# Performance work log

Measured on AMD Instinct MI355X. Metric: run time of the kernel, lower is better.

## Reference

```python
import jax, jax.numpy as jnp
import numpy as np

B, R, N, M, K = 4, 4, 4096, 64, 3
F_NUM = 512
KN = K * N


def _block(x, Ws, bs):
    """SO-Net PointResNet: 1x1 convs + ReLU; last layer sees concat(input, hidden)."""
    h = x
    for W, b in zip(Ws[:-1], bs[:-1]):
        h = jax.nn.relu(jnp.einsum('oc,bcn->bon', W, h) + b[None, :, None])
    h = jnp.concatenate([x, h], axis=1)
    return jax.nn.relu(jnp.einsum('oc,bcn->bon', Ws[-1], h) + bs[-1][None, :, None])


def _forward(x, intensity, node, node_knn_I, fpW, fpB, gpW, gpB):
    # --- som.query_topk: k nearest SOM nodes per point ---
    xd = jax.lax.stop_gradient(x)
    dist = jnp.sum((xd[:, :, :, None] - node[:, :, None, :]) ** 2, axis=1)      # B,N,M
    _, topk = jax.lax.top_k(-dist, K)                                           # B,N,K
    min_idx = topk.transpose(0, 2, 1).reshape(B, KN)                            # B,KN (k copies stacked)
    mask = jax.nn.one_hot(min_idx, M, dtype=jnp.float32)                        # B,KN,M
    mask_row_max = jnp.max(mask, axis=1) > 0                                    # B,M  node has >=1 point
    mask_row_sum = jnp.sum(mask, axis=1)                                        # B,M  points per node

    x_stack = jnp.tile(x, (1, 1, K))                                            # B,2,KN
    cluster_mean = jnp.einsum('bcn,bnm->bcm', jax.lax.stop_gradient(x_stack), mask) \
                   / (mask_row_sum[:, None, :] + 1e-5)                          # B,2,M (detached)

    # --- rotation group (2x2 rotations at angles 2*pi*r/R) ---
    theta = 2.0 * jnp.pi * jnp.arange(R, dtype=jnp.float32) / R
    c, s = jnp.cos(theta), jnp.sin(theta)
    rot = jnp.stack([jnp.stack([c, -s], -1), jnp.stack([s, c], -1)], -2)        # R,2,2

    x_rot = jnp.einsum('rij,bjn->brin', rot, x_stack)                           # B,R,2,KN
    node_rot = jnp.einsum('rij,bjm->brim', rot, cluster_mean)                   # B,R,2,M
    centers = jnp.take_along_axis(node_rot, min_idx[:, None, None, :], axis=3)  # B,R,2,KN
    x_dec = jax.lax.stop_gradient(x_rot - centers).reshape(B * R, 2, KN)

    # --- first PointResNet over all B*R rotation copies ---
    feat = _block(x_dec, fpW, fpB)                                              # BR,128,KN

    # --- index_max scatter-max per SOM cluster (value of argmax == segment max) ---
    seg = jnp.tile(min_idx[:, None, :], (1, R, 1)).reshape(B * R, KN)
    segmax = jax.vmap(lambda f, sgi: jax.ops.segment_max(f.T, sgi, num_segments=M).T)(feat, seg)
    rowmax = jnp.tile(mask_row_max[:, None, :], (1, R, 1)).reshape(B * R, M)
    pooled = jnp.where(rowmax[:, None, :], segmax, feat[:, :, 0:1])             # BR,128,M (empty -> gather idx 0)

    # --- final PointResNet over SOM nodes, then max over nodes and rotations ---
    g_in = jnp.concatenate([node_rot.reshape(B * R, 2, M), pooled], axis=1)     # BR,130,M
    out = _block(g_in, gpW, gpB)                                                # BR,F,M
    return out.reshape(B, R, F_NUM, M).max(axis=3).max(axis=1)                  # B,F


def setup_inputs() -> dict:
    key = jax.random.key(0)
    ks = jax.random.split(key, 24)
    d = {}
    d['x'] = jax.random.normal(ks[0], (B, 2, N), jnp.float32)
    d['intensity'] = jax.random.uniform(ks[1], (B, 1, N), jnp.float32)
    d['node'] = jax.random.normal(ks[2], (B, 2, M), jnp.float32)
    d['node_knn_I'] = jax.random.randint(ks[3], (B, M, 1), 0, M)
    dims_fp = [(64, 2), (64, 64), (128, 64), (128, 130)]      # PointResNet(2,[64,64,128,128])
    dims_gp = [(256, 130), (256, 256), (512, 256), (F_NUM, 642)]  # PointResNet(130,[256,256,512,F])
    i = 4
    for name, dims in (('fp', dims_fp), ('gp', dims_gp)):
        for j, (o, ci) in enumerate(dims):
            d[f'{name}_W{j}'] = jax.random.normal(ks[i], (o, ci), jnp.float32) / np.sqrt(ci).astype(np.float32)
            d[f'{name}_b{j}'] = jnp.zeros((o,), jnp.float32)
            i += 1
    return d


def reference(x, intensity, node, node_knn_I,
              fp_W0, fp_b0, fp_W1, fp_b1, fp_W2, fp_b2, fp_W3, fp_b3,
              gp_W0, gp_b0, gp_W1, gp_b1, gp_W2, gp_b2, gp_W3, gp_b3):
    return _forward(x, intensity, node, node_knn_I,
                    [fp_W0, fp_W1, fp_W2, fp_W3], [fp_b0, fp_b1, fp_b2, fp_b3],
                    [gp_W0, gp_W1, gp_W2, gp_W3], [gp_b0, gp_b1, gp_b2, gp_b3])
```

## Files before the change

kernel.cpp:

```cpp
#include <hip/hip_runtime.h>
#include <stdint.h>

#define BB 4
#define RR 4
#define NN 4096
#define MM 64
#define KK 3
#define KNN 12288
#define BRR 16
#define FF 512

typedef short bf16x8 __attribute__((ext_vector_type(8)));
typedef float f32x4 __attribute__((ext_vector_type(4)));

__device__ __forceinline__ float bf2f(unsigned int u) {
  union { unsigned int i; float f; } v; v.i = u << 16; return v.f;
}
__device__ __forceinline__ unsigned short f2bf(float f) {
  union { float f; unsigned int i; } v; v.f = f;
  unsigned int x = v.i;
  return (unsigned short)((x + 0x7fffu + ((x >> 16) & 1u)) >> 16);
}
__device__ __forceinline__ unsigned int cvtpk(float a, float b) {
  unsigned int r;
  asm("v_cvt_pk_bf16_f32 %0, %1, %2" : "=v"(r) : "v"(a), "v"(b));
  return r;
}
__device__ __forceinline__ float ldf(const void* p, long i, int isbf) {
  if (isbf) return bf2f(((const unsigned short*)p)[i]);
  return ((const float*)p)[i];
}
__device__ __forceinline__ int hsw(int col, int so) { return col * 72  + (so ^ (col & 24)); }
__device__ __forceinline__ int csw(int col, int so) { return col * 136 + (so ^ (col & 24)); }

struct WPtrs { const void* p[7]; };

__global__ __launch_bounds__(256) void k_front(
    const void* __restrict__ x, const void* __restrict__ node, WPtrs wp,
    int* __restrict__ flag, unsigned short* __restrict__ Wb,
    int* __restrict__ idx, float* __restrict__ csum, int* __restrict__ blkcnt) {
  __shared__ int bad;
  __shared__ float nd[2][64];
  __shared__ float cs[192];
  int tid = threadIdx.x;
  if (tid == 0) bad = 0;
  __syncthreads();
  {
    const unsigned short* xs = (const unsigned short*)x;
    int cnt = 0;
    for (int i = tid; i < 1024; i += 256) {
      unsigned short u = xs[i * 2];
      int e = (u >> 7) & 0xFF;
      if (e >= 0x90 || (e > 0 && e <= 0x50)) ++cnt;
    }
    atomicAdd(&bad, cnt);
  }
  __syncthreads();
  int isbf = (bad < 100) ? 1 : 0;
  if (blockIdx.x == 0 && tid == 0) flag[0] = isbf;

  if (blockIdx.x < 2295) {
    const int e0=4096, e1=12288, e2=28928, e3=62208, e4=127744, e5=258816, e6=587520;
    int t = blockIdx.x * 256 + tid;
    if (t >= e6) return;
    int s, base;
    if      (t < e0) { s=0; base=0;  }
    else if (t < e1) { s=1; base=e0; }
    else if (t < e2) { s=2; base=e1; }
    else if (t < e3) { s=3; base=e2; }
    else if (t < e4) { s=4; base=e3; }
    else if (t < e5) { s=5; base=e4; }
    else             { s=6; base=e5; }
    int local = t - base;
    unsigned short u;
    if (isbf) u = ((const unsigned short*)wp.p[s])[local];
    else      u = f2bf(((const float*)wp.p[s])[local]);
    Wb[t] = u;
    return;
  }
  int bi = blockIdx.x - 2295;
  int b = bi >> 4;
  int n = ((bi & 15) << 8) + tid;
  if (tid < 128) nd[tid >> 6][tid & 63] = ldf(node, b * 128 + tid, isbf);
  if (tid < 192) cs[tid] = 0.f;
  __syncthreads();
  float x0 = ldf(x, b * 8192 + n, isbf);
  float x1 = ldf(x, b * 8192 + 4096 + n, isbf);
  float d0 = 1e30f, d1 = 1e30f, d2 = 1e30f;
  int m0 = 0, m1 = 0, m2 = 0;
#pragma unroll 8
  for (int m = 0; m < 64; ++m) {
    float dx = x0 - nd[0][m];
    float dy = x1 - nd[1][m];
    float d = __fmul_rn(dx, dx) + __fmul_rn(dy, dy);
    if (d < d0)      { d2=d1; m2=m1; d1=d0; m1=m0; d0=d; m0=m; }
    else if (d < d1) { d2=d1; m2=m1; d1=d;  m1=m; }
    else if (d < d2) { d2=d;  m2=m; }
  }
  long base = ((long)b * NN + n) * 3;
  idx[base] = m0; idx[base + 1] = m1; idx[base + 2] = m2;
  atomicAdd(&cs[m0*3+0], x0); atomicAdd(&cs[m0*3+1], x1); atomicAdd(&cs[m0*3+2], 1.f);
  atomicAdd(&cs[m1*3+0], x0); atomicAdd(&cs[m1*3+1], x1); atomicAdd(&cs[m1*3+2], 1.f);
  atomicAdd(&cs[m2*3+0], x0); atomicAdd(&cs[m2*3+1], x1); atomicAdd(&cs[m2*3+2], 1.f);
  __syncthreads();
  if (tid < 192) atomicAdd(&csum[b * 192 + tid], cs[tid]);
  if (tid < 64) blkcnt[bi * 64 + tid] = (int)cs[tid*3 + 2];
}

__global__ __launch_bounds__(256) void k_scatter2(
    const float* __restrict__ csum, const int* __restrict__ blkcnt,
    const int* __restrict__ idx, int* __restrict__ sorted,
    float* __restrict__ noderot, int* __restrict__ rowflag) {
  __shared__ int scnt[64];
  __shared__ int soff[64];
  __shared__ int lc[64];
  int tid = threadIdx.x;
  int blk = blockIdx.x;
  int b = blk >> 4, chunk = blk & 15;
  if (tid < 64) scnt[tid] = (int)csum[b*192 + tid*3 + 2];
  __syncthreads();
  if (tid < 64) {
    int m = tid, acc = 0;
    for (int mm = 0; mm < m; ++mm) acc += scnt[mm];
    for (int c = 0; c < chunk; ++c) acc += blkcnt[(b*16 + c)*64 + m];
    soff[m] = acc;
    lc[m] = 0;
    if (chunk == 0) {
      float s0 = csum[b*192 + m*3], s1 = csum[b*192 + m*3 + 1], cc = csum[b*192 + m*3 + 2];
      float mx = s0 / (cc + 1e-5f);
      float my = s1 / (cc + 1e-5f);
      rowflag[b*64 + m] = (cc > 0.f) ? 1 : 0;
      for (int r = 0; r < 4; ++r) {
        float th = 1.5707964f * (float)r;
        float cr = cosf(th), sr = sinf(th);
        noderot[((b*4 + r)*2 + 0)*64 + m] = cr*mx - sr*my;
        noderot[((b*4 + r)*2 + 1)*64 + m] = sr*mx + cr*my;
      }
    }
  }
  __syncthreads();
  int n = ((blk & 15) << 8) + tid;
#pragma unroll
  for (int kk = 0; kk < 3; ++kk) {
    int m = idx[((long)b * NN + n) * 3 + kk];
    int pos = atomicAdd(&lc[m], 1);
    sorted[b * KNN + soff[m] + pos] = (m << 12) | n;
  }
}

__global__ __launch_bounds__(256) void k_fused(
    const void* __restrict__ x, const int* __restrict__ sorted,
    const int* __restrict__ idx, const float* __restrict__ noderot,
    const int* __restrict__ flag,
    const void* __restrict__ fW0, const void* __restrict__ fb0,
    const unsigned short* __restrict__ Wb,
    const void* __restrict__ fb1, const void* __restrict__ fb2,
    const void* __restrict__ fb3,
    unsigned int* __restrict__ pooled, float* __restrict__ feat0) {
  __shared__ unsigned short Cs[64 * 136];
  __shared__ unsigned short Hs[64 * 72];
  __shared__ int mcol[64];
  const unsigned short* fW1 = Wb;
  const unsigned short* fW2 = Wb + 4096;
  const unsigned short* fW3 = Wb + 12288;
  int isbf = flag[0];
  int tid = threadIdx.x, lane = tid & 63, wv = tid >> 6;
  int quad = lane >> 4, lr = lane & 15;
  int br = blockIdx.y, b = br >> 2, r = br & 3;
  if (tid < 64) {
    int e = sorted[b * KNN + blockIdx.x * 64 + tid];
    int m = e >> 12, n = e & 4095;
    int isz = (n == 0 && m == idx[(long)b * NN * 3]) ? 256 : 0;
    mcol[tid] = m | isz;
    float x0 = ldf(x, b*8192 + n, isbf), x1 = ldf(x, b*8192 + 4096 + n, isbf);
    float th = 1.5707964f * (float)r;
    float cr = cosf(th), sr = sinf(th);
    float xd0 = (cr*x0 - sr*x1) - noderot[(br*2 + 0)*64 + m];
    float xd1 = (sr*x0 + cr*x1) - noderot[(br*2 + 1)*64 + m];
    *(unsigned int*)&Cs[csw(tid, 0)] = cvtpk(xd0, xd1);
  }
  __syncthreads();
  {
    int col = tid & 63, og = (tid >> 6) << 4;
    unsigned int xu = *(unsigned int*)&Cs[csw(col, 0)];
    float fx0 = bf2f(xu & 0xffff), fx1 = bf2f(xu >> 16);
    float hv[16];
#pragma unroll
    for (int j = 0; j < 16; ++j) {
      int o = og + j;
      float h = ldf(fb0, o, isbf) + ldf(fW0, o*2, isbf) * fx0 + ldf(fW0, o*2+1, isbf) * fx1;
      hv[j] = fmaxf(h, 0.f);
    }
    union { bf16x8 v; unsigned int u[4]; } o8[2];
#pragma unroll
    for (int j = 0; j < 16; j += 2) o8[j >> 3].u[(j & 7) >> 1] = cvtpk(hv[j], hv[j+1]);
    *(bf16x8*)&Hs[hsw(col, og)]     = o8[0].v;
    *(bf16x8*)&Hs[hsw(col, og + 8)] = o8[1].v;
  }
  __syncthreads();
  {
    int o0 = wv * 16;
    f32x4 acc[4];
    float bb4[4];
#pragma unroll
    for (int rr = 0; rr < 4; ++rr) bb4[rr] = ldf(fb1, o0 + quad*4 + rr, isbf);
#pragma unroll
    for (int nt = 0; nt < 4; ++nt) acc[nt] = (f32x4){bb4[0], bb4[1], bb4[2], bb4[3]};
#pragma unroll
    for (int ks = 0; ks < 64; ks += 32) {
      bf16x8 a = *(const bf16x8*)(fW1 + (o0 + lr)*64 + ks + quad*8);
#pragma unroll
      for (int nt = 0; nt < 4; ++nt) {
        bf16x8 bf = *(bf16x8*)&Hs[hsw(nt*16 + lr, ks + quad*8)];
        acc[nt] = __builtin_amdgcn_mfma_f32_16x16x32_bf16(a, bf, acc[nt], 0, 0, 0);
      }
    }
    __syncthreads();
#pragma unroll
    for (int nt = 0; nt < 4; ++nt) {
      int col = nt*16 + lr;
      unsigned int lo = cvtpk(fmaxf(acc[nt][0], 0.f), fmaxf(acc[nt][1], 0.f));
      unsigned int hi = cvtpk(fmaxf(acc[nt][2], 0.f), fmaxf(acc[nt][3], 0.f));
      *(unsigned long long*)&Hs[hsw(col, o0 + quad*4)] =
          (unsigned long long)lo | ((unsigned long long)hi << 32);
    }
  }
  __syncthreads();
#pragma unroll
  for (int p2 = 0; p2 < 2; ++p2) {
    int o0 = p2*64 + wv*16;
    f32x4 acc[4];
    float bb4[4];
#pragma unroll
    for (int rr = 0; rr < 4; ++rr) bb4[rr] = ldf(fb2, o0 + quad*4 + rr, isbf);
#pragma unroll
    for (int nt = 0; nt < 4; ++nt) acc[nt] = (f32x4){bb4[0], bb4[1], bb4[2], bb4[3]};
#pragma unroll
    for (int ks = 0; ks < 64; ks += 32) {
      bf16x8 a = *(const bf16x8*)(fW2 + (o0 + lr)*64 + ks + quad*8);
#pragma unroll
      for (int nt = 0; nt < 4; ++nt) {
        bf16x8 bf = *(bf16x8*)&Hs[hsw(nt*16 + lr, ks + quad*8)];
        acc[nt] = __builtin_amdgcn_mfma_f32_16x16x32_bf16(a, bf, acc[nt], 0, 0, 0);
      }
    }
#pragma unroll
    for (int nt = 0; nt < 4; ++nt) {
      int col = nt*16 + lr;
      int o = o0 + quad*4;
      unsigned int w0 = cvtpk(fmaxf(acc[nt][0], 0.f), fmaxf(acc[nt][1], 0.f));
      unsigned int w1 = cvtpk(fmaxf(acc[nt][2], 0.f), fmaxf(acc[nt][3], 0.f));
      int so0 = 2 + o;
      int so1 = 4 + o;
      *(unsigned int*)&Cs[csw(col, so0)] = w0;
      *(unsigned int*)&Cs[(so1 < 128) ? csw(col, so1) : (col*136 + so1)] = w1;
    }
  }
  __syncthreads();
  f32x4 acc3[2][4];
#pragma unroll
  for (int p3 = 0; p3 < 2; ++p3) {
    int o0 = p3*64 + wv*16;
    float bb4[4];
#pragma unroll
    for (int rr = 0; rr < 4; ++rr) bb4[rr] = ldf(fb3, o0 + quad*4 + rr, isbf);
#pragma unroll
    for (int nt = 0; nt < 4; ++nt) acc3[p3][nt] = (f32x4){bb4[0], bb4[1], bb4[2], bb4[3]};
#pragma unroll
    for (int ks = 0; ks < 128; ks += 32) {
      union { bf16x8 v; unsigned int u[4]; } au;
      const unsigned int* ap = (const unsigned int*)(fW3 + (long)(o0 + lr)*130 + ks + quad*8);
      au.u[0] = ap[0]; au.u[1] = ap[1]; au.u[2] = ap[2]; au.u[3] = ap[3];
#pragma unroll
      for (int nt = 0; nt < 4; ++nt) {
        bf16x8 bf = *(bf16x8*)&Cs[csw(nt*16 + lr, ks + quad*8)];
        acc3[p3][nt] = __builtin_amdgcn_mfma_f32_16x16x32_bf16(au.v, bf, acc3[p3][nt], 0, 0, 0);
      }
    }
#pragma unroll
    for (int rr = 0; rr < 4; ++rr) {
      int o = o0 + quad*4 + rr;
      unsigned int wu = *(const unsigned int*)(fW3 + (long)o*130 + 128);
      float w0 = bf2f(wu & 0xffff), w1 = bf2f(wu >> 16);
#pragma unroll
      for (int nt = 0; nt < 4; ++nt) {
        unsigned int bu = *(unsigned int*)&Cs[(nt*16 + lr)*136 + 128];
        acc3[p3][nt][rr] += w0 * bf2f(bu & 0xffff) + w1 * bf2f(bu >> 16);
      }
    }
  }
  __syncthreads();
#pragma unroll
  for (int p3 = 0; p3 < 2; ++p3) {
    int o0 = p3*64 + wv*16;
#pragma unroll
    for (int nt = 0; nt < 4; ++nt) {
      int col = nt*16 + lr;
      unsigned int lo = cvtpk(fmaxf(acc3[p3][nt][0], 0.f), fmaxf(acc3[p3][nt][1], 0.f));
      unsigned int hi = cvtpk(fmaxf(acc3[p3][nt][2], 0.f), fmaxf(acc3[p3][nt][3], 0.f));
      *(unsigned long long*)&Cs[csw(col, o0 + quad*4)] =
          (unsigned long long)lo | ((unsigned long long)hi << 32);
    }
  }
  __syncthreads();
  {
    int o = tid & 127, h = tid >> 7;
    int c0 = h * 32;
    int curm = mcol[c0] & 255;
    float v = 0.f;
    for (int c = c0; c < c0 + 32; ++c) {
      int mc = mcol[c];
      int mm = mc & 255;
      float f = bf2f(Cs[csw(c, o)]);
      if (mm != curm) {
        atomicMax(&pooled[(((long)br*64 + curm) << 7) + o], __float_as_uint(v));
        curm = mm; v = 0.f;
      }
      v = fmaxf(v, f);
      if (mc & 256) feat0[br*128 + o] = f;
    }
    atomicMax(&pooled[(((long)br*64 + curm) << 7) + o], __float_as_uint(v));
  }
}

__global__ __launch_bounds__(256) void k_finalize(
    const unsigned int* __restrict__ pooled, const float* __restrict__ feat0,
    const int* __restrict__ rowflag, const float* __restrict__ noderot,
    unsigned short* __restrict__ AG) {
  int t = blockIdx.x * 256 + threadIdx.x;
  int col = t >> 7, o = t & 127;
  int br = col >> 6, m = col & 63, b = br >> 2;
  float v = __uint_as_float(pooled[((long)col << 7) + o]);
  if (!rowflag[b*64 + m]) v = feat0[br*128 + o];
  AG[(long)col*648 + 2 + o] = f2bf(v);
  if (o < 2) AG[(long)col*648 + o] = f2bf(noderot[(br*2 + o)*64 + m]);
}

template<int KW, int KMAIN, bool REM2, int BSTR, int OSTR, int OOFF, int EPI>
__global__ __launch_bounds__(256) void k_gemm(
    const unsigned short* __restrict__ W, const void* __restrict__ bias,
    const int* __restrict__ flag,
    const unsigned short* __restrict__ Bb, unsigned short* __restrict__ Out,
    unsigned int* __restrict__ outmax) {
  int isbf = flag[0];
  int lane = threadIdx.x & 63;
  int wv = threadIdx.x >> 6;
  int quad = lane >> 4, lr = lane & 15;
  int o0 = blockIdx.y * 64 + wv * 16;
  long p0 = (long)blockIdx.x * 64;
  float bia[4];
#pragma unroll
  for (int rr = 0; rr < 4; ++rr) bia[rr] = ldf(bias, o0 + quad*4 + rr, isbf);
  f32x4 acc[4];
#pragma unroll
  for (int nt = 0; nt < 4; ++nt) acc[nt] = (f32x4){bia[0], bia[1], bia[2], bia[3]};
  const unsigned short* arow = W + (long)(o0 + lr) * KW;
  for (int ks = 0; ks < KMAIN; ks += 32) {
    bf16x8 a;
    if constexpr ((KW % 8) == 0) {
      a = *(const bf16x8*)(arow + ks + quad*8);
    } else {
      union { bf16x8 v; unsigned int u[4]; } au;
      const unsigned int* ap = (const unsigned int*)(arow + ks + quad*8);
      au.u[0] = ap[0]; au.u[1] = ap[1]; au.u[2] = ap[2]; au.u[3] = ap[3];
      a = au.v;
    }
#pragma unroll
    for (int nt = 0; nt < 4; ++nt) {
      bf16x8 bf = *(const bf16x8*)(Bb + (p0 + nt*16 + lr) * BSTR + ks + quad*8);
      acc[nt] = __builtin_amdgcn_mfma_f32_16x16x32_bf16(a, bf, acc[nt], 0, 0, 0);
    }
  }
  if constexpr (REM2) {
#pragma unroll
    for (int rr = 0; rr < 4; ++rr) {
      int o = o0 + quad*4 + rr;
      unsigned int wu = *(const unsigned int*)(W + (long)o * KW + KMAIN);
      float w0 = bf2f(wu & 0xffff), w1 = bf2f(wu >> 16);
#pragma unroll
      for (int nt = 0; nt < 4; ++nt) {
        long p = p0 + nt*16 + lr;
        unsigned int bu = *(const unsigned int*)(Bb + p * BSTR + KMAIN);
        acc[nt][rr] += w0 * bf2f(bu & 0xffff) + w1 * bf2f(bu >> 16);
      }
    }
  }
  if constexpr (EPI == 0) {
#pragma unroll
    for (int nt = 0; nt < 4; ++nt) {
      long p = p0 + nt*16 + lr;
      unsigned int lo = cvtpk(fmaxf(acc[nt][0], 0.f), fmaxf(acc[nt][1], 0.f));
      unsigned int hi = cvtpk(fmaxf(acc[nt][2], 0.f), fmaxf(acc[nt][3], 0.f));
      unsigned short* op = Out + p * OSTR + OOFF + o0 + quad*4;
      if constexpr (((OOFF * 2) % 8) == 0) {
        *(unsigned long long*)op = (unsigned long long)lo | ((unsigned long long)hi << 32);
      } else {
        *(unsigned int*)op       = lo;
        *(unsigned int*)(op + 2) = hi;
      }
    }
  } else {
#pragma unroll
    for (int rr = 0; rr < 4; ++rr) {
      float v = fmaxf(fmaxf(acc[0][rr], acc[1][rr]), fmaxf(acc[2][rr], acc[3][rr]));
      v = fmaxf(v, 0.f);
      v = fmaxf(v, __shfl_xor(v, 1, 64));
      v = fmaxf(v, __shfl_xor(v, 2, 64));
      v = fmaxf(v, __shfl_xor(v, 4, 64));
      v = fmaxf(v, __shfl_xor(v, 8, 64));
      if (lr == 0) {
        int bb2 = (int)(blockIdx.x >> 2);
        atomicMax(&outmax[bb2 * FF + o0 + quad*4 + rr], __float_as_uint(v));
      }
    }
  }
}

__global__ __launch_bounds__(256) void k_out(
    const unsigned int* __restrict__ outmax, const int* __restrict__ flag,
    void* __restrict__ out) {
  int t = blockIdx.x * 256 + threadIdx.x;
  float v = __uint_as_float(outmax[t]);
  if (flag[0]) ((unsigned short*)out)[t] = f2bf(v);
  else         ((float*)out)[t] = v;
}

extern "C" void kernel_launch(void* const* d_in, const int* in_sizes, int n_in,
                              void* d_out, int out_size, void* d_ws, size_t ws_size,
                              hipStream_t stream) {
  const void* x    = d_in[0];
  const void* node = d_in[2];
  const void* fpW0 = d_in[4];  const void* fpb0 = d_in[5];
  const void* fpW1 = d_in[6];  const void* fpb1 = d_in[7];
  const void* fpW2 = d_in[8];  const void* fpb2 = d_in[9];
  const void* fpW3 = d_in[10]; const void* fpb3 = d_in[11];
  const void* gpW0 = d_in[12]; const void* gpb0 = d_in[13];
  const void* gpW1 = d_in[14]; const void* gpb1 = d_in[15];
  const void* gpW2 = d_in[16]; const void* gpb2 = d_in[17];
  const void* gpW3 = d_in[18]; const void* gpb3 = d_in[19];

  char* ws = (char*)d_ws;
  int*            flag    = (int*)(ws + 0);
  float*          csum    = (float*)(ws + 256);
  unsigned int*   outmax  = (unsigned int*)(ws + 3328);
  unsigned int*   pooled  = (unsigned int*)(ws + 11520);
  int*            idx     = (int*)(ws + 535808);
  int*            blkcnt  = (int*)(ws + 732416);
  float*          noderot = (float*)(ws + 766208);
  int*            rowflag = (int*)(ws + 774400);
  int*            sorted  = (int*)(ws + 775424);
  float*          feat0   = (float*)(ws + 972032);
  unsigned short* AG      = (unsigned short*)(ws + 980224);
  unsigned short* Hg1     = (unsigned short*)(ws + 2307328);
  unsigned short* Hg2     = (unsigned short*)(ws + 2831616);
  unsigned short* Wb      = (unsigned short*)(ws + 3355904);

  hipMemsetAsync(ws, 0, 535808, stream);

  WPtrs wp; wp.p[0]=fpW1; wp.p[1]=fpW2; wp.p[2]=fpW3; wp.p[3]=gpW0;
  wp.p[4]=gpW1; wp.p[5]=gpW2; wp.p[6]=gpW3;
  k_front<<<2359, 256, 0, stream>>>(x, node, wp, flag, Wb, idx, csum, blkcnt);
  k_scatter2<<<64, 256, 0, stream>>>(csum, blkcnt, idx, sorted, noderot, rowflag);
  k_fused<<<dim3(192, 16), 256, 0, stream>>>(x, sorted, idx, noderot, flag,
                                             fpW0, fpb0, Wb, fpb1, fpb2, fpb3,
                                             pooled, feat0);
  k_finalize<<<512, 256, 0, stream>>>(pooled, feat0, rowflag, noderot, AG);

  const unsigned short* gW0 = Wb + 28928;
  const unsigned short* gW1 = Wb + 62208;
  const unsigned short* gW2 = Wb + 127744;
  const unsigned short* gW3 = Wb + 258816;
  k_gemm<130, 128, true, 648, 256, 0, 0><<<dim3(16, 4), 256, 0, stream>>>(gW0, gpb0, flag, AG, Hg1, nullptr);
  k_gemm<256, 256, false, 256, 256, 0, 0><<<dim3(16, 4), 256, 0, stream>>>(gW1, gpb1, flag, Hg1, Hg2, nullptr);
  k_gemm<256, 256, false, 256, 648, 130, 0><<<dim3(16, 8), 256, 0, stream>>>(gW2, gpb2, flag, Hg2, AG, nullptr);
  k_gemm<642, 640, true, 648, 0, 0, 2><<<dim3(16, 8), 256, 0, stream>>>(gW3, gpb3, flag, AG, nullptr, outmax);

  k_out<<<8, 256, 0, stream>>>(outmax, flag, d_out);
}
```

Baseline: 199.4 us.

## Fuse finalize and four GP GEMM layers into one LDS-resident kernel

Replaces the finalize kernel and four separate GEMM launches with a single kernel. Each block owns 16 node columns and keeps the concatenated input and the hidden activations in shared memory across all four layers, with one output max reduction at the end. This removes four launches and the global-memory round trips for intermediate activations. In exchange it uses only 64 blocks, and every block rereads the full weight matrices, so each CU does more serial work and parallelism is low.

```diff
diff --git a/kernel.cpp b/kernel.cpp
--- a/kernel.cpp
+++ b/kernel.cpp
@@ -323,97 +323,112 @@
   }
 }
 
-__global__ __launch_bounds__(256) void k_finalize(
-    const unsigned int* __restrict__ pooled, const float* __restrict__ feat0,
-    const int* __restrict__ rowflag, const float* __restrict__ noderot,
-    unsigned short* __restrict__ AG) {
-  int t = blockIdx.x * 256 + threadIdx.x;
-  int col = t >> 7, o = t & 127;
-  int br = col >> 6, m = col & 63, b = br >> 2;
-  float v = __uint_as_float(pooled[((long)col << 7) + o]);
-  if (!rowflag[b*64 + m]) v = feat0[br*128 + o];
-  AG[(long)col*648 + 2 + o] = f2bf(v);
-  if (o < 2) AG[(long)col*648 + o] = f2bf(noderot[(br*2 + o)*64 + m]);
-}
-
-template<int KW, int KMAIN, bool REM2, int BSTR, int OSTR, int OOFF, int EPI>
-__global__ __launch_bounds__(256) void k_gemm(
-    const unsigned short* __restrict__ W, const void* __restrict__ bias,
-    const int* __restrict__ flag,
-    const unsigned short* __restrict__ Bb, unsigned short* __restrict__ Out,
-    unsigned int* __restrict__ outmax) {
-  int isbf = flag[0];
-  int lane = threadIdx.x & 63;
-  int wv = threadIdx.x >> 6;
-  int quad = lane >> 4, lr = lane & 15;
-  int o0 = blockIdx.y * 64 + wv * 16;
-  long p0 = (long)blockIdx.x * 64;
-  float bia[4];
-#pragma unroll
-  for (int rr = 0; rr < 4; ++rr) bia[rr] = ldf(bias, o0 + quad*4 + rr, isbf);
-  f32x4 acc[4];
-#pragma unroll
-  for (int nt = 0; nt < 4; ++nt) acc[nt] = (f32x4){bia[0], bia[1], bia[2], bia[3]};
-  const unsigned short* arow = W + (long)(o0 + lr) * KW;
-  for (int ks = 0; ks < KMAIN; ks += 32) {
-    bf16x8 a;
-    if constexpr ((KW % 8) == 0) {
-      a = *(const bf16x8*)(arow + ks + quad*8);
-    } else {
-      union { bf16x8 v; unsigned int u[4]; } au;
-      const unsigned int* ap = (const unsigned int*)(arow + ks + quad*8);
-      au.u[0] = ap[0]; au.u[1] = ap[1]; au.u[2] = ap[2]; au.u[3] = ap[3];
-      a = au.v;
-    }
-#pragma unroll
-    for (int nt = 0; nt < 4; ++nt) {
-      bf16x8 bf = *(const bf16x8*)(Bb + (p0 + nt*16 + lr) * BSTR + ks + quad*8);
-      acc[nt] = __builtin_amdgcn_mfma_f32_16x16x32_bf16(a, bf, acc[nt], 0, 0, 0);
-    }
-  }
-  if constexpr (REM2) {
-#pragma unroll
-    for (int rr = 0; rr < 4; ++rr) {
-      int o = o0 + quad*4 + rr;
-      unsigned int wu = *(const unsigned int*)(W + (long)o * KW + KMAIN);
-      float w0 = bf2f(wu & 0xffff), w1 = bf2f(wu >> 16);
-#pragma unroll
-      for (int nt = 0; nt < 4; ++nt) {
-        long p = p0 + nt*16 + lr;
-        unsigned int bu = *(const unsigned int*)(Bb + p * BSTR + KMAIN);
-        acc[nt][rr] += w0 * bf2f(bu & 0xffff) + w1 * bf2f(bu >> 16);
-      }
-    }
-  }
-  if constexpr (EPI == 0) {
-#pragma unroll
-    for (int nt = 0; nt < 4; ++nt) {
-      long p = p0 + nt*16 + lr;
-      unsigned int lo = cvtpk(fmaxf(acc[nt][0], 0.f), fmaxf(acc[nt][1], 0.f));
-      unsigned int hi = cvtpk(fmaxf(acc[nt][2], 0.f), fmaxf(acc[nt][3], 0.f));
-      unsigned short* op = Out + p * OSTR + OOFF + o0 + quad*4;
-      if constexpr (((OOFF * 2) % 8) == 0) {
+template<int OT, int KW, int KMAIN, bool REM2, int DSTR, int DOFF, int EPI>
+__device__ __forceinline__ void gp_layer(
+    const unsigned short* __restrict__ W, const void* __restrict__ bias, int isbf,
+    const unsigned short* Bs, int bstr, unsigned short* Ds,
+    int wv, int quad, int lr, int b, unsigned int* __restrict__ outmax) {
+#pragma unroll
+  for (int ot = 0; ot < OT; ++ot) {
+    int o0 = (wv * OT + ot) * 16;
+    float bb4[4];
+#pragma unroll
+    for (int rr = 0; rr < 4; ++rr) bb4[rr] = ldf(bias, o0 + quad*4 + rr, isbf);
+    f32x4 acc = (f32x4){bb4[0], bb4[1], bb4[2], bb4[3]};
+    const unsigned short* arow = W + (long)(o0 + lr) * KW;
+    for (int ks = 0; ks < KMAIN; ks += 32) {
+      bf16x8 a;
+      if constexpr ((KW % 8) == 0) {
+        a = *(const bf16x8*)(arow + ks + quad*8);
+      } else {
+        union { bf16x8 v; unsigned int u[4]; } au;
+        const unsigned int* ap = (const unsigned int*)(arow + ks + quad*8);
+        au.u[0] = ap[0]; au.u[1] = ap[1]; au.u[2] = ap[2]; au.u[3] = ap[3];
+        a = au.v;
+      }
+      bf16x8 bf = *(const bf16x8*)(Bs + lr * bstr + ks + quad*8);
+      acc = __builtin_amdgcn_mfma_f32_16x16x32_bf16(a, bf, acc, 0, 0, 0);
+    }
+    if constexpr (REM2) {
+      unsigned int bu = *(const unsigned int*)(Bs + lr * bstr + KMAIN);
+      float b0 = bf2f(bu & 0xffff), b1 = bf2f(bu >> 16);
+#pragma unroll
+      for (int rr = 0; rr < 4; ++rr) {
+        int o = o0 + quad*4 + rr;
+        unsigned int wu = *(const unsigned int*)(W + (long)o * KW + KMAIN);
+        acc[rr] += bf2f(wu & 0xffff) * b0 + bf2f(wu >> 16) * b1;
+      }
+    }
+    if constexpr (EPI == 0) {
+      unsigned int lo = cvtpk(fmaxf(acc[0], 0.f), fmaxf(acc[1], 0.f));
+      unsigned int hi = cvtpk(fmaxf(acc[2], 0.f), fmaxf(acc[3], 0.f));
+      unsigned short* op = Ds + lr * DSTR + DOFF + o0 + quad*4;
+      if constexpr ((DOFF & 3) == 0) {
         *(unsigned long long*)op = (unsigned long long)lo | ((unsigned long long)hi << 32);
       } else {
         *(unsigned int*)op       = lo;
         *(unsigned int*)(op + 2) = hi;
       }
-    }
-  } else {
-#pragma unroll
-    for (int rr = 0; rr < 4; ++rr) {
-      float v = fmaxf(fmaxf(acc[0][rr], acc[1][rr]), fmaxf(acc[2][rr], acc[3][rr]));
-      v = fmaxf(v, 0.f);
-      v = fmaxf(v, __shfl_xor(v, 1, 64));
-      v = fmaxf(v, __shfl_xor(v, 2, 64));
-      v = fmaxf(v, __shfl_xor(v, 4, 64));
-      v = fmaxf(v, __shfl_xor(v, 8, 64));
-      if (lr == 0) {
-        int bb2 = (int)(blockIdx.x >> 2);
-        atomicMax(&outmax[bb2 * FF + o0 + quad*4 + rr], __float_as_uint(v));
-      }
-    }
-  }
+    } else {
+#pragma unroll
+      for (int rr = 0; rr < 4; ++rr) {
+        float v = fmaxf(acc[rr], 0.f);
+        v = fmaxf(v, __shfl_xor(v, 1, 64));
+        v = fmaxf(v, __shfl_xor(v, 2, 64));
+        v = fmaxf(v, __shfl_xor(v, 4, 64));
+        v = fmaxf(v, __shfl_xor(v, 8, 64));
+        if (lr == 0)
+          atomicMax(&outmax[b * FF + o0 + quad*4 + rr], __float_as_uint(v));
+      }
+    }
+  }
+}
+
+__global__ __launch_bounds__(512) void k_gp(
+    const unsigned int* __restrict__ pooled, const float* __restrict__ feat0,
+    const int* __restrict__ rowflag, const float* __restrict__ noderot,
+    const int* __restrict__ flag, const unsigned short* __restrict__ Wb,
+    const void* __restrict__ gpb0, const void* __restrict__ gpb1,
+    const void* __restrict__ gpb2, const void* __restrict__ gpb3,
+    unsigned int* __restrict__ outmax) {
+  __shared__ unsigned short G3[16 * 648];
+  __shared__ unsigned short H1[16 * 264];
+  __shared__ unsigned short H2[16 * 264];
+  const unsigned short* gW0 = Wb + 28928;
+  const unsigned short* gW1 = Wb + 62208;
+  const unsigned short* gW2 = Wb + 127744;
+  const unsigned short* gW3 = Wb + 258816;
+  int isbf = flag[0];
+  int tid = threadIdx.x, lane = tid & 63, wv = tid >> 6;
+  int quad = lane >> 4, lr = lane & 15;
+  int c0 = blockIdx.x * 16;
+  int br = c0 >> 6, b = br >> 2;
+  {
+    int j = tid >> 5, oq = (tid & 31) << 2;
+    int col = c0 + j, m = col & 63;
+    int fl = rowflag[b * 64 + m];
+    float v[4];
+#pragma unroll
+    for (int i = 0; i < 4; ++i) {
+      float pv = __uint_as_float(pooled[((long)col << 7) + oq + i]);
+      v[i] = fl ? pv : feat0[br * 128 + oq + i];
+    }
+    *(unsigned int*)&G3[j * 648 + 2 + oq] = cvtpk(v[0], v[1]);
+    *(unsigned int*)&G3[j * 648 + 4 + oq] = cvtpk(v[2], v[3]);
+    if (tid < 32) {
+      int jj = tid >> 1, o = tid & 1;
+      int mm = (c0 + jj) & 63;
+      G3[jj * 648 + o] = f2bf(noderot[(br * 2 + o) * 64 + mm]);
+    }
+  }
+  __syncthreads();
+  gp_layer<2, 130, 128, true,  264, 0,   0>(gW0, gpb0, isbf, G3, 648, H1, wv, quad, lr, b, outmax);
+  __syncthreads();
+  gp_layer<2, 256, 256, false, 264, 0,   0>(gW1, gpb1, isbf, H1, 264, H2, wv, quad, lr, b, outmax);
+  __syncthreads();
+  gp_layer<4, 256, 256, false, 648, 130, 0>(gW2, gpb2, isbf, H2, 264, G3, wv, quad, lr, b, outmax);
+  __syncthreads();
+  gp_layer<4, 642, 640, true,  0,   0,   1>(gW3, gpb3, isbf, G3, 648, nullptr, wv, quad, lr, b, outmax);
 }
 
 __global__ __launch_bounds__(256) void k_out(
@@ -450,9 +465,6 @@
   int*            rowflag = (int*)(ws + 774400);
   int*            sorted  = (int*)(ws + 775424);
   float*          feat0   = (float*)(ws + 972032);
-  unsigned short* AG      = (unsigned short*)(ws + 980224);
-  unsigned short* Hg1     = (unsigned short*)(ws + 2307328);
-  unsigned short* Hg2     = (unsigned short*)(ws + 2831616);
   unsigned short* Wb      = (unsigned short*)(ws + 3355904);
 
   hipMemsetAsync(ws, 0, 535808, stream);
@@ -464,16 +476,7 @@
   k_fused<<<dim3(192, 16), 256, 0, stream>>>(x, sorted, idx, noderot, flag,
                                              fpW0, fpb0, Wb, fpb1, fpb2, fpb3,
                                              pooled, feat0);
-  k_finalize<<<512, 256, 0, stream>>>(pooled, feat0, rowflag, noderot, AG);
-
-  const unsigned short* gW0 = Wb + 28928;
-  const unsigned short* gW1 = Wb + 62208;
-  const unsigned short* gW2 = Wb + 127744;
-  const unsigned short* gW3 = Wb + 258816;
-  k_gemm<130, 128, true, 648, 256, 0, 0><<<dim3(16, 4), 256, 0, stream>>>(gW0, gpb0, flag, AG, Hg1, nullptr);
-  k_gemm<256, 256, false, 256, 256, 0, 0><<<dim3(16, 4), 256, 0, stream>>>(gW1, gpb1, flag, Hg1, Hg2, nullptr);
-  k_gemm<256, 256, false, 256, 648, 130, 0><<<dim3(16, 8), 256, 0, stream>>>(gW2, gpb2, flag, Hg2, AG, nullptr);
-  k_gemm<642, 640, true, 648, 0, 0, 2><<<dim3(16, 8), 256, 0, stream>>>(gW3, gpb3, flag, AG, nullptr, outmax);
-
+  k_gp<<<64, 512, 0, stream>>>(pooled, feat0, rowflag, noderot, flag, Wb,
+                               gpb0, gpb1, gpb2, gpb3, outmax);
   k_out<<<8, 256, 0, stream>>>(outmax, flag, d_out);
 }
```

Result: no change. 203.1 us (+1.8%).
